# Performance work log

Measured on AMD Instinct MI355X. Metric: run time of the kernel, lower is better.

Reference implementation:

```python
import jax, jax.numpy as jnp
import numpy as np

H = 8          # num heads
LN_EPS = 1e-5  # torch LayerNorm default

_SHAPES = {
    'src': (1024, 8, 256), 'pos': (1024, 8, 256), 'query_embed': (80, 8, 256), 'cam_mask': (8, 80, 1024),
    'enc_qkv_w': (2, 768, 256), 'enc_qkv_b': (2, 768), 'enc_out_w': (2, 256, 256), 'enc_out_b': (2, 256),
    'enc_ln1_g': (2, 256), 'enc_ln1_b': (2, 256),
    'enc_ff1_w': (2, 2048, 256), 'enc_ff1_b': (2, 2048), 'enc_ff2_w': (2, 256, 2048), 'enc_ff2_b': (2, 256),
    'enc_ln2_g': (2, 256), 'enc_ln2_b': (2, 256),
    'dec_sa_qkv_w': (2, 768, 256), 'dec_sa_qkv_b': (2, 768), 'dec_sa_out_w': (2, 256, 256), 'dec_sa_out_b': (2, 256),
    'dec_ln1_g': (2, 256), 'dec_ln1_b': (2, 256),
    'dec_ca_qkv_w': (2, 768, 256), 'dec_ca_qkv_b': (2, 768), 'dec_ca_out_w': (2, 256, 256), 'dec_ca_out_b': (2, 256),
    'dec_ln2_g': (2, 256), 'dec_ln2_b': (2, 256),
    'dec_ff1_w': (2, 2048, 256), 'dec_ff1_b': (2, 2048), 'dec_ff2_w': (2, 256, 2048), 'dec_ff2_b': (2, 256),
    'dec_ln3_g': (2, 256), 'dec_ln3_b': (2, 256),
    'dec_norm_g': (256,), 'dec_norm_b': (256,),
}


def setup_inputs() -> dict:
    key = jax.random.key(0)
    out = {}
    for i, (name, sh) in enumerate(_SHAPES.items()):
        k = jax.random.fold_in(key, i)
        if name.endswith('_g'):
            out[name] = jnp.ones(sh, jnp.float32)
        elif name.endswith('ln1_b') or name.endswith('ln2_b') or name.endswith('ln3_b') or name == 'dec_norm_b':
            out[name] = jnp.zeros(sh, jnp.float32)
        else:
            scale = 1.0 if name in ('src', 'pos', 'query_embed', 'cam_mask') else 0.02
            out[name] = jax.random.normal(k, sh, dtype=jnp.float32) * scale
    return out


def layer_norm(x, g, b):
    mu = jnp.mean(x, axis=-1, keepdims=True)
    var = jnp.mean(jnp.square(x - mu), axis=-1, keepdims=True)
    return (x - mu) * jax.lax.rsqrt(var + LN_EPS) * g + b


def mha(q_in, k_in, v_in, qkv_w, qkv_b, out_w, out_b, bias=None):
    # q_in: [L,B,D], k_in/v_in: [S,B,D]; torch layout: projections are x @ W.T + b
    L, B, D = q_in.shape
    S = k_in.shape[0]
    hd = D // H
    wq, wk, wv = qkv_w[:D], qkv_w[D:2 * D], qkv_w[2 * D:]
    bq, bk, bv = qkv_b[:D], qkv_b[D:2 * D], qkv_b[2 * D:]
    q = (q_in @ wq.T + bq).reshape(L, B, H, hd).transpose(1, 2, 0, 3)  # [B,H,L,hd]
    k = (k_in @ wk.T + bk).reshape(S, B, H, hd).transpose(1, 2, 0, 3)  # [B,H,S,hd]
    v = (v_in @ wv.T + bv).reshape(S, B, H, hd).transpose(1, 2, 0, 3)
    logits = jnp.einsum('bhld,bhsd->bhls', q, k) * (1.0 / np.sqrt(hd))
    if bias is not None:
        logits = logits + bias[:, None, :, :]  # CAM bias broadcast over heads
    attn = jax.nn.softmax(logits, axis=-1)
    o = jnp.einsum('bhls,bhsd->bhld', attn, v).transpose(2, 0, 1, 3).reshape(L, B, D)
    return o @ out_w.T + out_b


def reference(src, pos, query_embed, cam_mask,
              enc_qkv_w, enc_qkv_b, enc_out_w, enc_out_b, enc_ln1_g, enc_ln1_b,
              enc_ff1_w, enc_ff1_b, enc_ff2_w, enc_ff2_b, enc_ln2_g, enc_ln2_b,
              dec_sa_qkv_w, dec_sa_qkv_b, dec_sa_out_w, dec_sa_out_b, dec_ln1_g, dec_ln1_b,
              dec_ca_qkv_w, dec_ca_qkv_b, dec_ca_out_w, dec_ca_out_b, dec_ln2_g, dec_ln2_b,
              dec_ff1_w, dec_ff1_b, dec_ff2_w, dec_ff2_b, dec_ln3_g, dec_ln3_b,
              dec_norm_g, dec_norm_b):
    n_enc = enc_qkv_w.shape[0]
    n_dec = dec_sa_qkv_w.shape[0]
    # --- encoder (post-norm DETR style, pos added to q,k) ---
    mem = src
    for i in range(n_enc):
        qk = mem + pos
        a = mha(qk, qk, mem, enc_qkv_w[i], enc_qkv_b[i], enc_out_w[i], enc_out_b[i])
        mem = layer_norm(mem + a, enc_ln1_g[i], enc_ln1_b[i])
        f = jax.nn.relu(mem @ enc_ff1_w[i].T + enc_ff1_b[i]) @ enc_ff2_w[i].T + enc_ff2_b[i]
        mem = layer_norm(mem + f, enc_ln2_g[i], enc_ln2_b[i])
    # --- decoder: tgt starts at zeros (Q2L), query_embed is query_pos ---
    tgt = jnp.zeros_like(query_embed)
    for i in range(n_dec):
        qk = tgt + query_embed
        sa = mha(qk, qk, tgt, dec_sa_qkv_w[i], dec_sa_qkv_b[i], dec_sa_out_w[i], dec_sa_out_b[i])
        tgt = layer_norm(tgt + sa, dec_ln1_g[i], dec_ln1_b[i])
        ca = mha(tgt + query_embed, mem + pos, mem,
                 dec_ca_qkv_w[i], dec_ca_qkv_b[i], dec_ca_out_w[i], dec_ca_out_b[i],
                 bias=cam_mask)  # MA: CAM-derived additive attention bias [B,L,S]
        tgt = layer_norm(tgt + ca, dec_ln2_g[i], dec_ln2_b[i])
        f = jax.nn.relu(tgt @ dec_ff1_w[i].T + dec_ff1_b[i]) @ dec_ff2_w[i].T + dec_ff2_b[i]
        tgt = layer_norm(tgt + f, dec_ln3_g[i], dec_ln3_b[i])
    out = layer_norm(tgt, dec_norm_g, dec_norm_b)
    return out[None]  # [1, L, B, D] as in TransformerDecoder's output.unsqueeze(0)
```

## Files before the change

### kernel.cpp

```cpp
#include <hip/hip_runtime.h>
#include <hip/hip_bf16.h>
#include <cstdint>
#include <cstddef>

typedef __hip_bfloat16 bf16;
typedef float f4 __attribute__((ext_vector_type(4)));
typedef float f32x4 __attribute__((ext_vector_type(4)));
typedef short s8v __attribute__((ext_vector_type(8)));
typedef unsigned short u16x4 __attribute__((ext_vector_type(4)));
typedef unsigned short u16x8 __attribute__((ext_vector_type(8)));

#define LN_EPS 1e-5f
#define LOG2E 1.4426950408889634f

#if __has_builtin(__builtin_amdgcn_exp2f)
__device__ __forceinline__ float EXP2(float x) { return __builtin_amdgcn_exp2f(x); }
#else
__device__ __forceinline__ float EXP2(float x) {
  float r; asm("v_exp_f32 %0, %1" : "=v"(r) : "v"(x)); return r;
}
#endif

__device__ __forceinline__ void async_cp16(const void* g, void* lds) {
  __builtin_amdgcn_global_load_lds(
      (const __attribute__((address_space(1))) unsigned int*)g,
      (__attribute__((address_space(3))) unsigned int*)lds, 16, 0, 0);
}

__device__ __forceinline__ uint32_t pkbf(float lo, float hi) {
#if __has_builtin(__builtin_amdgcn_perm)
  uint32_t l = __builtin_bit_cast(uint32_t, lo) + 0x8000u;
  uint32_t h = __builtin_bit_cast(uint32_t, hi) + 0x8000u;
  return __builtin_amdgcn_perm(h, l, 0x07060302u);
#else
  uint32_t l = __builtin_bit_cast(uint32_t, lo) + 0x8000u;
  uint32_t h = __builtin_bit_cast(uint32_t, hi) + 0x8000u;
  return (l >> 16) | (h & 0xFFFF0000u);
#endif
}

#define NCAST 17
struct CastArgs {
  const float* in[NCAST];
  bf16* out[NCAST];
  int end4[NCAST];
  int nseg;
};

__global__ __launch_bounds__(256) void cast_multi(CastArgs a, int total4) {
  int i = blockIdx.x * 256 + threadIdx.x;
  if (i >= total4) return;
  int s = 0;
  while (i >= a.end4[s]) ++s;
  int j = i - (s ? a.end4[s - 1] : 0);
  f4 v = ((const f4*)a.in[s])[j];
  u16x4 o;
#pragma unroll
  for (int c = 0; c < 4; ++c) {
    bf16 h = __float2bfloat16(v[c]);
    o[c] = *reinterpret_cast<unsigned short*>(&h);
  }
  ((u16x4*)a.out[s])[j] = o;
}

__global__ __launch_bounds__(256) void scale_f32_kernel(const float* __restrict__ in,
                                                        float* __restrict__ out,
                                                        float s, int n4) {
  int i = blockIdx.x * 256 + threadIdx.x;
  if (i < n4) {
    f4 v = ((const f4*)in)[i];
    ((f4*)out)[i] = v * s;
  }
}

__global__ __launch_bounds__(256) void add_bf16_kernel(const float* __restrict__ a,
                                                       const float* __restrict__ b,
                                                       bf16* __restrict__ out, int n4) {
  int i = blockIdx.x * 256 + threadIdx.x;
  if (i < n4) {
    f4 x = ((const f4*)a)[i];
    f4 y = ((const f4*)b)[i];
    u16x4 o;
#pragma unroll
    for (int j = 0; j < 4; ++j) {
      bf16 h = __float2bfloat16(x[j] + y[j]);
      o[j] = *reinterpret_cast<unsigned short*>(&h);
    }
    ((u16x4*)out)[i] = o;
  }
}

template <int TB, int MODE, int SPLITK>
__global__ __launch_bounds__(256, 2) void mfma_gemm(
    const bf16* __restrict__ A, const bf16* __restrict__ W,
    const float* __restrict__ bias, float* __restrict__ C,
    bf16* __restrict__ Cb, int M, int N, int K, int HL, float qscale) {
  constexpr int WM = TB / 2, WN = TB / 2;
  constexpr int MR = WM / 16, NR = WN / 16;
  constexpr int NCH = TB / 32;
  __shared__ __attribute__((aligned(16))) unsigned short SH[TB * 128];
  unsigned short (*As)[64] = (unsigned short(*)[64])SH;
  unsigned short (*Ws)[64] = (unsigned short(*)[64])(SH + TB * 64);
  const int tid = threadIdx.x;
  const int lane = tid & 63, wave = tid >> 6;
  const int wr = wave >> 1, wc = wave & 1;
  const int bm = blockIdx.x * TB, bn = blockIdx.y * TB;
  const int fr = lane & 15, fo = lane >> 4;
  const int srowi = lane >> 3;
  const int slot = lane & 7;
  const int gcol = (slot ^ srowi) * 8;

  const int kchunk = K / SPLITK;
  const int kbeg = (SPLITK > 1) ? blockIdx.z * kchunk : 0;

  f32x4 acc[MR][NR] = {};

  for (int k0 = kbeg; k0 < kbeg + kchunk; k0 += 64) {
    __syncthreads();
#pragma unroll
    for (int c = 0; c < NCH; ++c) {
      int rbase = wave * (TB / 4) + c * 8;
      int row = rbase + srowi;
      async_cp16(A + (size_t)(bm + row) * K + k0 + gcol, &As[rbase][0]);
      async_cp16(W + (size_t)(bn + row) * K + k0 + gcol, &Ws[rbase][0]);
    }
    __syncthreads();
#pragma unroll
    for (int ks = 0; ks < 2; ++ks) {
      s8v a[MR], b[NR];
#pragma unroll
      for (int mi = 0; mi < MR; ++mi) {
        int row = wr * WM + mi * 16 + fr;
        a[mi] = *(const s8v*)((const char*)&As[0][0] + row * 128 +
                              ((ks * 64 + fo * 16) ^ ((row & 7) << 4)));
      }
#pragma unroll
      for (int ni = 0; ni < NR; ++ni) {
        int row = wc * WN + ni * 16 + fr;
        b[ni] = *(const s8v*)((const char*)&Ws[0][0] + row * 128 +
                              ((ks * 64 + fo * 16) ^ ((row & 7) << 4)));
      }
#pragma unroll
      for (int mi = 0; mi < MR; ++mi)
#pragma unroll
        for (int ni = 0; ni < NR; ++ni)
          acc[mi][ni] = __builtin_amdgcn_mfma_f32_16x16x32_bf16(
              a[mi], b[ni], acc[mi][ni], 0, 0, 0);
    }
  }

  const int r0 = (lane >> 4) * 4;

  if (MODE == 5) {
    __syncthreads();
    unsigned short (*T)[72] = (unsigned short(*)[72])SH;
#pragma unroll
    for (int mi = 0; mi < MR; ++mi)
#pragma unroll
      for (int ni = 0; ni < NR; ++ni) {
        int colL = wc * WN + ni * 16 + fr;
        float bv = bias[bn + colL];
#pragma unroll
        for (int r = 0; r < 4; ++r) {
          int rowL = wr * WM + mi * 16 + r0 + r;
          bf16 hv = __float2bfloat16(acc[mi][ni][r] + bv);
          T[colL][rowL] = *(unsigned short*)&hv;
        }
      }
    __syncthreads();
    const int lbase = bm >> 3;
#pragma unroll
    for (int jj = 0; jj < 2; ++jj) {
      int cid = tid * 2 + jj;
      int colL = cid >> 3, bb = cid & 7;
      int c = bn + colL;
      int sec = c >> 8, hh = (c >> 5) & 7, d = c & 31;
      u16x8 v;
#pragma unroll
      for (int l = 0; l < 8; ++l) v[l] = T[colL][bb + 8 * l];
      *(u16x8*)(Cb + (size_t)sec * ((size_t)64 * 32 * HL) +
                ((size_t)(bb * 8 + hh) * 32 + d) * HL + lbase) = v;
    }
    return;
  }

  float* Cz = (MODE == 4) ? C + (size_t)blockIdx.z * M * N : C;
#pragma unroll
  for (int mi = 0; mi < MR; ++mi) {
#pragma unroll
    for (int ni = 0; ni < NR; ++ni) {
      int col = bn + wc * WN + ni * 16 + fr;
      float bv = (MODE == 4) ? 0.f : bias[col];
#pragma unroll
      for (int r = 0; r < 4; ++r) {
        int row = bm + wr * WM + mi * 16 + r0 + r;
        float t = acc[mi][ni][r] + bv;
        if (MODE == 2) t = fmaxf(t, 0.f);
        if (MODE == 0) {
          C[(size_t)row * N + col] = t;
        } else if (MODE == 4) {
          Cz[(size_t)row * N + col] = t;
        } else if (MODE == 3) {
          int l = row >> 3, bb = row & 7;
          int sec = col >> 8, hh = (col >> 5) & 7, d = col & 31;
          if (sec == 0) t *= qscale;
          Cb[(size_t)sec * ((size_t)64 * HL * 32) +
             ((size_t)(bb * 8 + hh) * HL + l) * 32 + d] = __float2bfloat16(t);
        } else {
          Cb[(size_t)row * N + col] = __float2bfloat16(t);
        }
      }
    }
  }
}

template <int HAS_BIAS, int PARTIAL, int NW>
__global__ __launch_bounds__(NW * 64, 3) void attn_mfma(
    const bf16* __restrict__ Qh, const bf16* __restrict__ Kh,
    const bf16* __restrict__ VhT, const float* __restrict__ bias,
    bf16* __restrict__ O, float* __restrict__ PO, float* __restrict__ PM,
    float* __restrict__ PL, int L, int S, int SC) {
  __shared__ __attribute__((aligned(16))) uint32_t Ps2[NW][2][16][36];
  const int tid = threadIdx.x;
  const int lane = tid & 63, wave = tid >> 6;
  const int fr = lane & 15, fo = lane >> 4;
  const int bh = blockIdx.x;
  const int b = bh >> 3, h = bh & 7;
  const int q0 = blockIdx.y * (NW * 16) + wave * 16;
  const int q = q0 + fr;

  const int cz = PARTIAL ? blockIdx.z : 0;
  const int sb = PARTIAL ? cz * SC : 0;
  const int se = PARTIAL ? min(S, sb + SC) : S;
  const int ng = (se - sb + 63) >> 6;

  s8v qf = {};
  if (q < L) qf = *(const s8v*)(Qh + ((size_t)bh * L + q) * 32 + fo * 8);

  const float* brow = nullptr;
  if (HAS_BIAS) brow = bias + ((size_t)b * L + (q < L ? q : L - 1)) * S;

  const bf16* Kbase = Kh + (size_t)bh * S * 32;
  const bf16* Vbase = VhT + (size_t)bh * 32 * S;

  float mA = -1e30f, lsA = 0.f, mB = -1e30f, lsB = 0.f;
  f32x4 oA[2] = {}, oB[2] = {};

  for (int g = 0; g < ng; g += 2) {
    const int sA = sb + g * 64, sB = sA + 64;

    s8v kA[4], kB[4], vA[2][2], vB[2][2];
#pragma unroll
    for (int kb = 0; kb < 4; ++kb) {
      kA[kb] = *(const s8v*)(Kbase + (size_t)(sA + kb * 16 + fr) * 32 + fo * 8);
      kB[kb] = *(const s8v*)(Kbase + (size_t)(sB + kb * 16 + fr) * 32 + fo * 8);
    }
#pragma unroll
    for (int dh = 0; dh < 2; ++dh)
#pragma unroll
      for (int ks = 0; ks < 2; ++ks) {
        vA[dh][ks] = *(const s8v*)(Vbase + (size_t)(dh * 16 + fr) * S +
                                   sA + ks * 32 + fo * 8);
        vB[dh][ks] = *(const s8v*)(Vbase + (size_t)(dh * 16 + fr) * S +
                                   sB + ks * 32 + fo * 8);
      }
    f4 bA[4], bB[4];
    if (HAS_BIAS) {
#pragma unroll
      for (int kb = 0; kb < 4; ++kb) {
        bA[kb] = *(const f4*)(brow + sA + kb * 16 + 4 * fo);
        bB[kb] = *(const f4*)(brow + sB + kb * 16 + 4 * fo);
      }
    }

    float lgA[16], lgB[16];
    __builtin_amdgcn_s_setprio(1);
#pragma unroll
    for (int kb = 0; kb < 4; ++kb) {
      f32x4 z = {};
      f32x4 sa = __builtin_amdgcn_mfma_f32_16x16x32_bf16(kA[kb], qf, z, 0, 0, 0);
#pragma unroll
      for (int r = 0; r < 4; ++r) lgA[kb * 4 + r] = sa[r];
    }
#pragma unroll
    for (int kb = 0; kb < 4; ++kb) {
      f32x4 z = {};
      f32x4 sa = __builtin_amdgcn_mfma_f32_16x16x32_bf16(kB[kb], qf, z, 0, 0, 0);
#pragma unroll
      for (int r = 0; r < 4; ++r) lgB[kb * 4 + r] = sa[r];
    }
    __builtin_amdgcn_s_setprio(0);
    if (HAS_BIAS) {
#pragma unroll
      for (int i = 0; i < 16; ++i) { lgA[i] += bA[i >> 2][i & 3]; lgB[i] += bB[i >> 2][i & 3]; }
    }
    if (sB + 64 > se) {
#pragma unroll
      for (int i = 0; i < 16; ++i) {
        int keyA = sA + (i >> 2) * 16 + 4 * fo + (i & 3);
        int keyB = sB + (i >> 2) * 16 + 4 * fo + (i & 3);
        if (keyA >= se) lgA[i] = -1e30f;
        if (keyB >= se) lgB[i] = -1e30f;
      }
    }

    float tA, tB;
    {
      float a0 = fmaxf(fmaxf(lgA[0], lgA[1]), fmaxf(lgA[2], lgA[3]));
      float a1 = fmaxf(fmaxf(lgA[4], lgA[5]), fmaxf(lgA[6], lgA[7]));
      float a2 = fmaxf(fmaxf(lgA[8], lgA[9]), fmaxf(lgA[10], lgA[11]));
      float a3 = fmaxf(fmaxf(lgA[12], lgA[13]), fmaxf(lgA[14], lgA[15]));
      tA = fmaxf(fmaxf(a0, a1), fmaxf(a2, a3));
      float b0 = fmaxf(fmaxf(lgB[0], lgB[1]), fmaxf(lgB[2], lgB[3]));
      float b1 = fmaxf(fmaxf(lgB[4], lgB[5]), fmaxf(lgB[6], lgB[7]));
      float b2 = fmaxf(fmaxf(lgB[8], lgB[9]), fmaxf(lgB[10], lgB[11]));
      float b3 = fmaxf(fmaxf(lgB[12], lgB[13]), fmaxf(lgB[14], lgB[15]));
      tB = fmaxf(fmaxf(b0, b1), fmaxf(b2, b3));
    }
    tA = fmaxf(tA, __shfl_xor(tA, 16));
    tB = fmaxf(tB, __shfl_xor(tB, 16));
    tA = fmaxf(tA, __shfl_xor(tA, 32));
    tB = fmaxf(tB, __shfl_xor(tB, 32));

    float nmA = fmaxf(mA, tA), nmB = fmaxf(mB, tB);
    float rsA = EXP2(mA - nmA), rsB = EXP2(mB - nmB);
    mA = nmA; mB = nmB;

    float psA = 0.f, psB = 0.f;
#pragma unroll
    for (int i = 0; i < 16; ++i) {
      lgA[i] = EXP2(lgA[i] - nmA); psA += lgA[i];
      lgB[i] = EXP2(lgB[i] - nmB); psB += lgB[i];
    }
    lsA = lsA * rsA + psA;
    lsB = lsB * rsB + psB;

#pragma unroll
    for (int kb = 0; kb < 4; ++kb) {
      uint32_t a0 = pkbf(lgA[kb * 4 + 0], lgA[kb * 4 + 1]);
      uint32_t a1 = pkbf(lgA[kb * 4 + 2], lgA[kb * 4 + 3]);
      *(uint64_t*)&Ps2[wave][0][fr][kb * 8 + 2 * fo] =
          (uint64_t)a0 | ((uint64_t)a1 << 32);
      uint32_t b0 = pkbf(lgB[kb * 4 + 0], lgB[kb * 4 + 1]);
      uint32_t b1 = pkbf(lgB[kb * 4 + 2], lgB[kb * 4 + 3]);
      *(uint64_t*)&Ps2[wave][1][fr][kb * 8 + 2 * fo] =
          (uint64_t)b0 | ((uint64_t)b1 << 32);
    }

#pragma unroll
    for (int r = 0; r < 4; ++r) {
      oA[0][r] *= rsA; oA[1][r] *= rsA;
      oB[0][r] *= rsB; oB[1][r] *= rsB;
    }
    s8v pA[2], pB[2];
#pragma unroll
    for (int ks = 0; ks < 2; ++ks) {
      pA[ks] = *(const s8v*)&Ps2[wave][0][fr][ks * 16 + 4 * fo];
      pB[ks] = *(const s8v*)&Ps2[wave][1][fr][ks * 16 + 4 * fo];
    }
    __builtin_amdgcn_s_setprio(1);
#pragma unroll
    for (int dh = 0; dh < 2; ++dh)
#pragma unroll
      for (int ks = 0; ks < 2; ++ks) {
        oA[dh] = __builtin_amdgcn_mfma_f32_16x16x32_bf16(vA[dh][ks], pA[ks], oA[dh], 0, 0, 0);
        oB[dh] = __builtin_amdgcn_mfma_f32_16x16x32_bf16(vB[dh][ks], pB[ks], oB[dh], 0, 0, 0);
      }
    __builtin_amdgcn_s_setprio(0);
  }

  float m = fmaxf(mA, mB);
  float wA = EXP2(mA - m), wB = EXP2(mB - m);
  float lsum = lsA * wA + lsB * wB;
  f32x4 oacc[2];
#pragma unroll
  for (int dh = 0; dh < 2; ++dh)
#pragma unroll
    for (int r = 0; r < 4; ++r)
      oacc[dh][r] = oA[dh][r] * wA + oB[dh][r] * wB;

  lsum += __shfl_xor(lsum, 16);
  lsum += __shfl_xor(lsum, 32);

  if (q < L) {
    if (PARTIAL) {
      size_t pi = ((size_t)cz * 64 + bh) * L + q;
      float* po = PO + pi * 32;
#pragma unroll
      for (int dh = 0; dh < 2; ++dh) {
        f4 t2;
#pragma unroll
        for (int r = 0; r < 4; ++r) t2[r] = oacc[dh][r];
        *(f4*)(po + dh * 16 + 4 * fo) = t2;
      }
      if (fo == 0) { PM[pi] = m; PL[pi] = lsum; }
    } else {
      float inv = 1.f / lsum;
      bf16* op = O + ((size_t)q * 8 + b) * 256 + h * 32;
#pragma unroll
      for (int dh = 0; dh < 2; ++dh) {
        uint32_t w0 = pkbf(oacc[dh][0] * inv, oacc[dh][1] * inv);
        uint32_t w1 = pkbf(oacc[dh][2] * inv, oacc[dh][3] * inv);
        *(uint32_t*)(op + dh * 16 + 4 * fo) = w0;
        *(uint32_t*)(op + dh * 16 + 4 * fo + 2) = w1;
      }
    }
  }
}

__global__ __launch_bounds__(256) void attn_combine(
    const float* __restrict__ PO, const float* __restrict__ PM,
    const float* __restrict__ PL, bf16* __restrict__ O, int L, int NC) {
  int gid = blockIdx.x * 256 + threadIdx.x;
  if (gid >= 64 * L * 32) return;
  int d = gid & 31;
  int rem = gid >> 5;
  int q = rem % L, bh = rem / L;
  int b = bh >> 3, h = bh & 7;
  float M = -1e30f;
  for (int c = 0; c < NC; ++c) M = fmaxf(M, PM[((size_t)c * 64 + bh) * L + q]);
  float lsum = 0.f, o = 0.f;
  for (int c = 0; c < NC; ++c) {
    size_t pi = ((size_t)c * 64 + bh) * L + q;
    float w = EXP2(PM[pi] - M);
    lsum += PL[pi] * w;
    o += PO[pi * 32 + d] * w;
  }
  O[((size_t)q * 8 + b) * 256 + h * 32 + d] = __float2bfloat16(o / lsum);
}

__global__ __launch_bounds__(256) void ln_kernel(
    const float* __restrict__ x, const float* __restrict__ res,
    const float* __restrict__ parts, int nparts, int pstride,
    const float* __restrict__ gbias,
    const float* __restrict__ g, const float* __restrict__ b,
    float* __restrict__ out, bf16* __restrict__ outb,
    const float* __restrict__ aux, bf16* __restrict__ auxb) {
  const int row = blockIdx.x, tid = threadIdx.x;
  size_t idx = (size_t)row * 256 + tid;
  float v = x[idx];
  if (res) v += res[idx];
  if (parts) {
    for (int z = 0; z < nparts; ++z) v += parts[(size_t)z * pstride + idx];
  }
  if (gbias) v += gbias[tid];
  float s = v, s2 = v * v;
#pragma unroll
  for (int off = 32; off >= 1; off >>= 1) {
    s += __shfl_down(s, off);
    s2 += __shfl_down(s2, off);
  }
  __shared__ float red[8];
  int wv = tid >> 6;
  if ((tid & 63) == 0) { red[wv] = s; red[4 + wv] = s2; }
  __syncthreads();
  if (tid == 0) {
    float ts = red[0] + red[1] + red[2] + red[3];
    float ts2 = red[4] + red[5] + red[6] + red[7];
    float mu = ts * (1.f / 256.f);
    float var = ts2 * (1.f / 256.f) - mu * mu;
    red[0] = mu;
    red[1] = rsqrtf(var + LN_EPS);
  }
  __syncthreads();
  float y = (v - red[0]) * red[1] * g[tid] + b[tid];
  if (out) out[idx] = y;
  if (outb) outb[idx] = __float2bfloat16(y);
  if (auxb) auxb[idx] = __float2bfloat16(y + aux[idx]);
}

extern "C" void kernel_launch(void* const* d_in, const int* in_sizes, int n_in,
                              void* d_out, int out_size, void* d_ws, size_t ws_size,
                              hipStream_t stream) {
  const float* src         = (const float*)d_in[0];
  const float* pos         = (const float*)d_in[1];
  const float* query_embed = (const float*)d_in[2];
  const float* cam_mask    = (const float*)d_in[3];
  const float* enc_qkv_w   = (const float*)d_in[4];
  const float* enc_qkv_b   = (const float*)d_in[5];
  const float* enc_out_w   = (const float*)d_in[6];
  const float* enc_out_b   = (const float*)d_in[7];
  const float* enc_ln1_g   = (const float*)d_in[8];
  const float* enc_ln1_b   = (const float*)d_in[9];
  const float* enc_ff1_w   = (const float*)d_in[10];
  const float* enc_ff1_b   = (const float*)d_in[11];
  const float* enc_ff2_w   = (const float*)d_in[12];
  const float* enc_ff2_b   = (const float*)d_in[13];
  const float* enc_ln2_g   = (const float*)d_in[14];
  const float* enc_ln2_b   = (const float*)d_in[15];
  const float* dec_sa_qkv_w= (const float*)d_in[16];
  const float* dec_sa_qkv_b= (const float*)d_in[17];
  const float* dec_sa_out_w= (const float*)d_in[18];
  const float* dec_sa_out_b= (const float*)d_in[19];
  const float* dec_ln1_g   = (const float*)d_in[20];
  const float* dec_ln1_b   = (const float*)d_in[21];
  const float* dec_ca_qkv_w= (const float*)d_in[22];
  const float* dec_ca_qkv_b= (const float*)d_in[23];
  const float* dec_ca_out_w= (const float*)d_in[24];
  const float* dec_ca_out_b= (const float*)d_in[25];
  const float* dec_ln2_g   = (const float*)d_in[26];
  const float* dec_ln2_b   = (const float*)d_in[27];
  const float* dec_ff1_w   = (const float*)d_in[28];
  const float* dec_ff1_b   = (const float*)d_in[29];
  const float* dec_ff2_w   = (const float*)d_in[30];
  const float* dec_ff2_b   = (const float*)d_in[31];
  const float* dec_ln3_g   = (const float*)d_in[32];
  const float* dec_ln3_b   = (const float*)d_in[33];
  const float* dec_norm_g  = (const float*)d_in[34];
  const float* dec_norm_b  = (const float*)d_in[35];

  size_t off = 0;
  char* base = (char*)d_ws;
  auto af = [&](size_t n) { float* p = (float*)(base + off); off += n * 4; return p; };
  auto ab = [&](size_t n) { bf16*  p = (bf16*)(base + off);  off += n * 2; return p; };

  float* mem  = af(2097152);
  float* r1   = af(2097152);
  float* PO   = af(8388608);
  float* pm   = af(262144);
  float* pl   = af(262144);
  float* cmlog= af(655360);
  float* pb   = af(1024);
  float* tgt  = af(163840);
  bf16* memb  = ab(2097152);
  bf16* qkb   = ab(2097152);
  bf16* aob   = ab(2097152);
  bf16* ffb   = ab(16777216);
  bf16* bufQ  = ab(4194304);
  bf16* bufK  = ab(4194304);
  bf16* bufV  = ab(4194304);
  bf16* bufVsa= ab(172032);
  bf16* tgtb  = ab(163840);
  bf16* tqkb  = ab(163840);
  bf16* taob  = ab(163840);
  bf16* qeb   = ab(163840);
  bf16* tffb  = ab(1310720);
  bf16* w_enc_qkv = ab(393216);
  bf16* w_enc_out = ab(131072);
  bf16* w_enc_ff1 = ab(1048576);
  bf16* w_enc_ff2 = ab(1048576);
  bf16* w_sa_qkv  = ab(393216);
  bf16* w_sa_out  = ab(131072);
  bf16* w_ca_q    = ab(131072);
  bf16* w_ca_kv   = ab(262144);
  bf16* w_ca_out  = ab(131072);
  bf16* w_dec_ff1 = ab(1048576);
  bf16* w_dec_ff2 = ab(1048576);

  const float qscale = 0.17677669529663687f * LOG2E;

  {
    CastArgs ca;
    const float* ins[NCAST] = {
        enc_qkv_w, enc_out_w, enc_ff1_w, enc_ff2_w,
        dec_sa_qkv_w, dec_sa_out_w,
        dec_ca_qkv_w,
        dec_ca_qkv_w + 65536,
        dec_ca_qkv_w + 131072,
        dec_ca_qkv_w + 196608,
        dec_ca_qkv_w + 262144,
        dec_ca_qkv_w + 327680,
        dec_ca_out_w, dec_ff1_w, dec_ff2_w, src, query_embed};
    bf16* outs[NCAST] = {
        w_enc_qkv, w_enc_out, w_enc_ff1, w_enc_ff2,
        w_sa_qkv, w_sa_out,
        w_ca_q,
        w_ca_kv,
        w_ca_kv + 131072,
        w_ca_q + 65536,
        w_ca_kv + 65536,
        w_ca_kv + 196608,
        w_ca_out, w_dec_ff1, w_dec_ff2, memb, qeb};
    int n4s[NCAST] = {98304, 32768, 262144, 262144, 98304, 32768,
                      16384, 16384, 16384, 16384, 16384, 16384,
                      32768, 262144, 262144, 524288, 40960};
    int acc = 0;
    for (int s = 0; s < NCAST; ++s) {
      ca.in[s] = ins[s]; ca.out[s] = outs[s];
      acc += n4s[s]; ca.end4[s] = acc;
    }
    ca.nseg = NCAST;
    cast_multi<<<(acc + 255) / 256, 256, 0, stream>>>(ca, acc);
  }
  scale_f32_kernel<<<640, 256, 0, stream>>>(cam_mask, cmlog, LOG2E, 163840);
  hipMemcpyAsync(mem, src, (size_t)2097152 * 4, hipMemcpyDeviceToDevice, stream);
  hipMemcpyAsync(pb,       dec_ca_qkv_b + 256,       1024, hipMemcpyDeviceToDevice, stream);
  hipMemcpyAsync(pb + 256, dec_ca_qkv_b + 768 + 256, 1024, hipMemcpyDeviceToDevice, stream);
  hipMemcpyAsync(pb + 512, dec_ca_qkv_b + 512,       1024, hipMemcpyDeviceToDevice, stream);
  hipMemcpyAsync(pb + 768, dec_ca_qkv_b + 768 + 512, 1024, hipMemcpyDeviceToDevice, stream);

  auto g64_head = [&](const bf16* A, const bf16* W, const float* bias, bf16* Cb,
                      int M, int N, int K, int HL, float qs) {
    mfma_gemm<64, 3, 1><<<dim3(M / 64, N / 64), 256, 0, stream>>>(
        A, W, bias, nullptr, Cb, M, N, K, HL, qs);
  };
  auto g64_headT = [&](const bf16* A, const bf16* W, const float* bias, bf16* Cb,
                       int M, int N, int K, int HL) {
    mfma_gemm<64, 5, 1><<<dim3(M / 64, N / 64), 256, 0, stream>>>(
        A, W, bias, nullptr, Cb, M, N, K, HL, 1.f);
  };
  auto g64_relu = [&](const bf16* A, const bf16* W, const float* bias, bf16* Cb,
                      int M, int N, int K) {
    mfma_gemm<64, 2, 1><<<dim3(M / 64, N / 64), 256, 0, stream>>>(
        A, W, bias, nullptr, Cb, M, N, K, 0, 1.f);
  };
  auto g128_relu = [&](const bf16* A, const bf16* W, const float* bias, bf16* Cb,
                       int M, int N, int K) {
    mfma_gemm<128, 2, 1><<<dim3(M / 128, N / 128), 256, 0, stream>>>(
        A, W, bias, nullptr, Cb, M, N, K, 0, 1.f);
  };

  add_bf16_kernel<<<2048, 256, 0, stream>>>(mem, pos, qkb, 524288);
  for (int i = 0; i < 2; ++i) {
    const bf16* wq = w_enc_qkv + (size_t)i * 196608;
    const float* qkvb = enc_qkv_b + (size_t)i * 768;
    g64_head(qkb, wq, qkvb, bufQ, 8192, 512, 256, 1024, qscale);
    g64_headT(memb, wq + 131072, qkvb + 512, bufV, 8192, 256, 256, 1024);
    attn_mfma<0, 0, 4><<<dim3(64, 16), 256, 0, stream>>>(
        bufQ, bufQ + 2097152, bufV, nullptr, aob, nullptr, nullptr, nullptr,
        1024, 1024, 0);
    mfma_gemm<64, 4, 2><<<dim3(128, 4, 2), 256, 0, stream>>>(
        aob, w_enc_out + (size_t)i * 65536, nullptr, PO, nullptr,
        8192, 256, 256, 0, 1.f);
    ln_kernel<<<8192, 256, 0, stream>>>(mem, nullptr, PO, 2, 2097152,
                                        enc_out_b + i * 256,
                                        enc_ln1_g + i * 256, enc_ln1_b + i * 256,
                                        mem, memb, nullptr, nullptr);
    g128_relu(memb, w_enc_ff1 + (size_t)i * 524288, enc_ff1_b + i * 2048, ffb,
              8192, 2048, 256);
    mfma_gemm<64, 4, 2><<<dim3(128, 4, 2), 256, 0, stream>>>(
        ffb, w_enc_ff2 + (size_t)i * 524288, nullptr, PO, nullptr,
        8192, 256, 2048, 0, 1.f);
    ln_kernel<<<8192, 256, 0, stream>>>(mem, nullptr, PO, 2, 2097152,
                                        enc_ff2_b + i * 256,
                                        enc_ln2_g + i * 256, enc_ln2_b + i * 256,
                                        mem, memb, pos, qkb);
  }

  hipMemsetAsync(tgt, 0, (size_t)163840 * 4, stream);
  hipMemsetAsync(tgtb, 0, (size_t)163840 * 2, stream);

  g64_head(qkb, w_ca_kv, pb, bufK, 8192, 512, 256, 1024, 1.f);
  g64_headT(memb, w_ca_kv + 131072, pb + 512, bufV, 8192, 512, 256, 1024);

  for (int i = 0; i < 2; ++i) {
    const bf16* wsa = w_sa_qkv + (size_t)i * 196608;
    const float* sab = dec_sa_qkv_b + (size_t)i * 768;
    const float* cab = dec_ca_qkv_b + (size_t)i * 768;
    const bf16* sa_in = (i == 0) ? qeb : tqkb;

    g64_head(sa_in, wsa, sab, bufQ, 640, 512, 256, 80, qscale);
    g64_headT(tgtb, wsa + 131072, sab + 512, bufVsa, 640, 256, 256, 80);
    attn_mfma<0, 0, 1><<<dim3(64, 5), 64, 0, stream>>>(
        bufQ, bufQ + 163840, bufVsa, nullptr, taob, nullptr, nullptr, nullptr,
        80, 80, 0);
    mfma_gemm<64, 4, 4><<<dim3(10, 4, 4), 256, 0, stream>>>(
        taob, w_sa_out + (size_t)i * 65536, nullptr, PO, nullptr,
        640, 256, 256, 0, 1.f);
    ln_kernel<<<640, 256, 0, stream>>>(tgt, nullptr, PO, 4, 163840,
                                       dec_sa_out_b + i * 256,
                                       dec_ln1_g + i * 256, dec_ln1_b + i * 256,
                                       tgt, tgtb, query_embed, tqkb);
    g64_head(tqkb, w_ca_q + (size_t)i * 65536, cab, bufQ, 640, 256, 256, 80, qscale);
    attn_mfma<1, 1, 1><<<dim3(64, 5, 8), 64, 0, stream>>>(
        bufQ, bufK + (size_t)i * 2097152, bufV + (size_t)i * 2097152, cmlog,
        nullptr, PO + 4194304, pm, pl, 80, 1024, 128);
    attn_combine<<<640, 256, 0, stream>>>(PO + 4194304, pm, pl, taob, 80, 8);
    mfma_gemm<64, 4, 4><<<dim3(10, 4, 4), 256, 0, stream>>>(
        taob, w_ca_out + (size_t)i * 65536, nullptr, PO, nullptr,
        640, 256, 256, 0, 1.f);
    ln_kernel<<<640, 256, 0, stream>>>(tgt, nullptr, PO, 4, 163840,
                                       dec_ca_out_b + i * 256,
                                       dec_ln2_g + i * 256, dec_ln2_b + i * 256,
                                       tgt, tgtb, nullptr, nullptr);
    g64_relu(tgtb, w_dec_ff1 + (size_t)i * 524288, dec_ff1_b + i * 2048, tffb,
             640, 2048, 256);
    mfma_gemm<64, 4, 4><<<dim3(10, 4, 4), 256, 0, stream>>>(
        tffb, w_dec_ff2 + (size_t)i * 524288, nullptr, PO, nullptr,
        640, 256, 2048, 0, 1.f);
    ln_kernel<<<640, 256, 0, stream>>>(tgt, nullptr, PO, 4, 163840,
                                       dec_ff2_b + i * 256,
                                       dec_ln3_g + i * 256, dec_ln3_b + i * 256,
                                       tgt, tgtb, query_embed, tqkb);
  }

  ln_kernel<<<640, 256, 0, stream>>>(tgt, nullptr, nullptr, 0, 0, nullptr,
                                     dec_norm_g, dec_norm_b,
                                     (float*)d_out, nullptr, nullptr, nullptr);
}
```

Measured before the change: 422.6 us.

## Fuse QK and V head projections into one launch; shortcut first decoder self-attention

A new GEMM mode 6 selects the A operand and output layout by column block, so the Q/K projection (head layout) and the V projection (transposed layout) run in a single launch for the encoder QKV, the cross-attention KV, and decoder layer-1 self-attention. For decoder layer 0, tgt is zero, so V equals its bias and attention output is the same for every query. The whole self-attention block therefore collapses to one row, out_w·bv + out_b followed by LayerNorm, which is broadcast to all rows. This removes several launches and the layer-0 self-attention GEMMs; it relies on the algebraic identity that holds for any inputs, since tgt starts at zero by model definition.

```diff
diff --git a/kernel.cpp b/kernel.cpp
--- a/kernel.cpp
+++ b/kernel.cpp
@@ -90,11 +90,56 @@
   }
 }
 
+__global__ __launch_bounds__(256) void sa0_row(
+    const float* __restrict__ Wo, const float* __restrict__ bv,
+    const float* __restrict__ bo, const float* __restrict__ g,
+    const float* __restrict__ b, float* __restrict__ row_out) {
+  const int j = threadIdx.x;
+  float acc = bo[j];
+  for (int k = 0; k < 256; k += 4) {
+    f4 w = *(const f4*)(Wo + (size_t)j * 256 + k);
+    f4 v = *(const f4*)(bv + k);
+    acc += w[0] * v[0] + w[1] * v[1] + w[2] * v[2] + w[3] * v[3];
+  }
+  float s = acc, s2 = acc * acc;
+#pragma unroll
+  for (int off = 32; off >= 1; off >>= 1) {
+    s += __shfl_down(s, off);
+    s2 += __shfl_down(s2, off);
+  }
+  __shared__ float red[8];
+  int wv = j >> 6;
+  if ((j & 63) == 0) { red[wv] = s; red[4 + wv] = s2; }
+  __syncthreads();
+  if (j == 0) {
+    float ts = red[0] + red[1] + red[2] + red[3];
+    float ts2 = red[4] + red[5] + red[6] + red[7];
+    float mu = ts * (1.f / 256.f);
+    float var = ts2 * (1.f / 256.f) - mu * mu;
+    red[0] = mu;
+    red[1] = rsqrtf(var + LN_EPS);
+  }
+  __syncthreads();
+  row_out[j] = (acc - red[0]) * red[1] * g[j] + b[j];
+}
+
+__global__ __launch_bounds__(256) void sa0_bcast(
+    const float* __restrict__ row, const float* __restrict__ qe,
+    float* __restrict__ tgt, bf16* __restrict__ tgtb, bf16* __restrict__ tqkb) {
+  const int r = blockIdx.x, j = threadIdx.x;
+  float y = row[j];
+  size_t idx = (size_t)r * 256 + j;
+  tgt[idx] = y;
+  tgtb[idx] = __float2bfloat16(y);
+  tqkb[idx] = __float2bfloat16(y + qe[idx]);
+}
+
 template <int TB, int MODE, int SPLITK>
 __global__ __launch_bounds__(256, 2) void mfma_gemm(
     const bf16* __restrict__ A, const bf16* __restrict__ W,
     const float* __restrict__ bias, float* __restrict__ C,
-    bf16* __restrict__ Cb, int M, int N, int K, int HL, float qscale) {
+    bf16* __restrict__ Cb, int M, int N, int K, int HL, float qscale,
+    const bf16* __restrict__ A2, bf16* __restrict__ Cb2, int nyA, int secV) {
   constexpr int WM = TB / 2, WN = TB / 2;
   constexpr int MR = WM / 16, NR = WN / 16;
   constexpr int NCH = TB / 32;
@@ -110,6 +155,8 @@
   const int slot = lane & 7;
   const int gcol = (slot ^ srowi) * 8;
 
+  const bf16* Aeff = (MODE == 6) ? (((int)blockIdx.y < nyA) ? A : A2) : A;
+
   const int kchunk = K / SPLITK;
   const int kbeg = (SPLITK > 1) ? blockIdx.z * kchunk : 0;
 
@@ -121,7 +168,7 @@
     for (int c = 0; c < NCH; ++c) {
       int rbase = wave * (TB / 4) + c * 8;
       int row = rbase + srowi;
-      async_cp16(A + (size_t)(bm + row) * K + k0 + gcol, &As[rbase][0]);
+      async_cp16(Aeff + (size_t)(bm + row) * K + k0 + gcol, &As[rbase][0]);
       async_cp16(W + (size_t)(bn + row) * K + k0 + gcol, &Ws[rbase][0]);
     }
     __syncthreads();
@@ -151,7 +198,7 @@
 
   const int r0 = (lane >> 4) * 4;
 
-  if (MODE == 5) {
+  if (MODE == 5 || (MODE == 6 && (bn >> 8) >= secV)) {
     __syncthreads();
     unsigned short (*T)[72] = (unsigned short(*)[72])SH;
 #pragma unroll
@@ -168,17 +215,19 @@
         }
       }
     __syncthreads();
+    bf16* Cv = (MODE == 6) ? Cb2 : Cb;
+    const int secBase = (MODE == 6) ? secV : 0;
     const int lbase = bm >> 3;
 #pragma unroll
     for (int jj = 0; jj < 2; ++jj) {
       int cid = tid * 2 + jj;
       int colL = cid >> 3, bb = cid & 7;
       int c = bn + colL;
-      int sec = c >> 8, hh = (c >> 5) & 7, d = c & 31;
+      int sec = (c >> 8) - secBase, hh = (c >> 5) & 7, d = c & 31;
       u16x8 v;
 #pragma unroll
       for (int l = 0; l < 8; ++l) v[l] = T[colL][bb + 8 * l];
-      *(u16x8*)(Cb + (size_t)sec * ((size_t)64 * 32 * HL) +
+      *(u16x8*)(Cv + (size_t)sec * ((size_t)64 * 32 * HL) +
                 ((size_t)(bb * 8 + hh) * 32 + d) * HL + lbase) = v;
     }
     return;
@@ -200,7 +249,7 @@
           C[(size_t)row * N + col] = t;
         } else if (MODE == 4) {
           Cz[(size_t)row * N + col] = t;
-        } else if (MODE == 3) {
+        } else if (MODE == 3 || MODE == 6) {
           int l = row >> 3, bb = row & 7;
           int sec = col >> 8, hh = (col >> 5) & 7, d = col & 31;
           if (sec == 0) t *= qscale;
@@ -515,12 +564,12 @@
   auto ab = [&](size_t n) { bf16*  p = (bf16*)(base + off);  off += n * 2; return p; };
 
   float* mem  = af(2097152);
-  float* r1   = af(2097152);
   float* PO   = af(8388608);
   float* pm   = af(262144);
   float* pl   = af(262144);
   float* cmlog= af(655360);
   float* pb   = af(1024);
+  float* row0 = af(256);
   float* tgt  = af(163840);
   bf16* memb  = ab(2097152);
   bf16* qkb   = ab(2097152);
@@ -592,36 +641,32 @@
   auto g64_head = [&](const bf16* A, const bf16* W, const float* bias, bf16* Cb,
                       int M, int N, int K, int HL, float qs) {
     mfma_gemm<64, 3, 1><<<dim3(M / 64, N / 64), 256, 0, stream>>>(
-        A, W, bias, nullptr, Cb, M, N, K, HL, qs);
-  };
-  auto g64_headT = [&](const bf16* A, const bf16* W, const float* bias, bf16* Cb,
-                       int M, int N, int K, int HL) {
-    mfma_gemm<64, 5, 1><<<dim3(M / 64, N / 64), 256, 0, stream>>>(
-        A, W, bias, nullptr, Cb, M, N, K, HL, 1.f);
+        A, W, bias, nullptr, Cb, M, N, K, HL, qs, nullptr, nullptr, 0, 0);
   };
   auto g64_relu = [&](const bf16* A, const bf16* W, const float* bias, bf16* Cb,
                       int M, int N, int K) {
     mfma_gemm<64, 2, 1><<<dim3(M / 64, N / 64), 256, 0, stream>>>(
-        A, W, bias, nullptr, Cb, M, N, K, 0, 1.f);
+        A, W, bias, nullptr, Cb, M, N, K, 0, 1.f, nullptr, nullptr, 0, 0);
   };
   auto g128_relu = [&](const bf16* A, const bf16* W, const float* bias, bf16* Cb,
                        int M, int N, int K) {
     mfma_gemm<128, 2, 1><<<dim3(M / 128, N / 128), 256, 0, stream>>>(
-        A, W, bias, nullptr, Cb, M, N, K, 0, 1.f);
+        A, W, bias, nullptr, Cb, M, N, K, 0, 1.f, nullptr, nullptr, 0, 0);
   };
 
   add_bf16_kernel<<<2048, 256, 0, stream>>>(mem, pos, qkb, 524288);
   for (int i = 0; i < 2; ++i) {
     const bf16* wq = w_enc_qkv + (size_t)i * 196608;
     const float* qkvb = enc_qkv_b + (size_t)i * 768;
-    g64_head(qkb, wq, qkvb, bufQ, 8192, 512, 256, 1024, qscale);
-    g64_headT(memb, wq + 131072, qkvb + 512, bufV, 8192, 256, 256, 1024);
+    mfma_gemm<64, 6, 1><<<dim3(128, 12), 256, 0, stream>>>(
+        qkb, wq, qkvb, nullptr, bufQ, 8192, 768, 256, 1024, qscale,
+        memb, bufV, 8, 2);
     attn_mfma<0, 0, 4><<<dim3(64, 16), 256, 0, stream>>>(
         bufQ, bufQ + 2097152, bufV, nullptr, aob, nullptr, nullptr, nullptr,
         1024, 1024, 0);
     mfma_gemm<64, 4, 2><<<dim3(128, 4, 2), 256, 0, stream>>>(
         aob, w_enc_out + (size_t)i * 65536, nullptr, PO, nullptr,
-        8192, 256, 256, 0, 1.f);
+        8192, 256, 256, 0, 1.f, nullptr, nullptr, 0, 0);
     ln_kernel<<<8192, 256, 0, stream>>>(mem, nullptr, PO, 2, 2097152,
                                         enc_out_b + i * 256,
                                         enc_ln1_g + i * 256, enc_ln1_b + i * 256,
@@ -630,37 +675,41 @@
               8192, 2048, 256);
     mfma_gemm<64, 4, 2><<<dim3(128, 4, 2), 256, 0, stream>>>(
         ffb, w_enc_ff2 + (size_t)i * 524288, nullptr, PO, nullptr,
-        8192, 256, 2048, 0, 1.f);
+        8192, 256, 2048, 0, 1.f, nullptr, nullptr, 0, 0);
     ln_kernel<<<8192, 256, 0, stream>>>(mem, nullptr, PO, 2, 2097152,
                                         enc_ff2_b + i * 256,
                                         enc_ln2_g + i * 256, enc_ln2_b + i * 256,
                                         mem, memb, pos, qkb);
   }
 
-  hipMemsetAsync(tgt, 0, (size_t)163840 * 4, stream);
-  hipMemsetAsync(tgtb, 0, (size_t)163840 * 2, stream);
-
-  g64_head(qkb, w_ca_kv, pb, bufK, 8192, 512, 256, 1024, 1.f);
-  g64_headT(memb, w_ca_kv + 131072, pb + 512, bufV, 8192, 512, 256, 1024);
+  mfma_gemm<64, 6, 1><<<dim3(128, 16), 256, 0, stream>>>(
+      qkb, w_ca_kv, pb, nullptr, bufK, 8192, 1024, 256, 1024, 1.f,
+      memb, bufV, 8, 2);
 
   for (int i = 0; i < 2; ++i) {
-    const bf16* wsa = w_sa_qkv + (size_t)i * 196608;
     const float* sab = dec_sa_qkv_b + (size_t)i * 768;
     const float* cab = dec_ca_qkv_b + (size_t)i * 768;
-    const bf16* sa_in = (i == 0) ? qeb : tqkb;
-
-    g64_head(sa_in, wsa, sab, bufQ, 640, 512, 256, 80, qscale);
-    g64_headT(tgtb, wsa + 131072, sab + 512, bufVsa, 640, 256, 256, 80);
-    attn_mfma<0, 0, 1><<<dim3(64, 5), 64, 0, stream>>>(
-        bufQ, bufQ + 163840, bufVsa, nullptr, taob, nullptr, nullptr, nullptr,
-        80, 80, 0);
-    mfma_gemm<64, 4, 4><<<dim3(10, 4, 4), 256, 0, stream>>>(
-        taob, w_sa_out + (size_t)i * 65536, nullptr, PO, nullptr,
-        640, 256, 256, 0, 1.f);
-    ln_kernel<<<640, 256, 0, stream>>>(tgt, nullptr, PO, 4, 163840,
-                                       dec_sa_out_b + i * 256,
-                                       dec_ln1_g + i * 256, dec_ln1_b + i * 256,
-                                       tgt, tgtb, query_embed, tqkb);
+
+    if (i == 0) {
+      sa0_row<<<1, 256, 0, stream>>>(dec_sa_out_w, dec_sa_qkv_b + 512,
+                                     dec_sa_out_b, dec_ln1_g, dec_ln1_b, row0);
+      sa0_bcast<<<640, 256, 0, stream>>>(row0, query_embed, tgt, tgtb, tqkb);
+    } else {
+      const bf16* wsa = w_sa_qkv + (size_t)i * 196608;
+      mfma_gemm<64, 6, 1><<<dim3(10, 12), 256, 0, stream>>>(
+          tqkb, wsa, sab, nullptr, bufQ, 640, 768, 256, 80, qscale,
+          tgtb, bufVsa, 8, 2);
+      attn_mfma<0, 0, 1><<<dim3(64, 5), 64, 0, stream>>>(
+          bufQ, bufQ + 163840, bufVsa, nullptr, taob, nullptr, nullptr, nullptr,
+          80, 80, 0);
+      mfma_gemm<64, 4, 4><<<dim3(10, 4, 4), 256, 0, stream>>>(
+          taob, w_sa_out + (size_t)i * 65536, nullptr, PO, nullptr,
+          640, 256, 256, 0, 1.f, nullptr, nullptr, 0, 0);
+      ln_kernel<<<640, 256, 0, stream>>>(tgt, nullptr, PO, 4, 163840,
+                                         dec_sa_out_b + i * 256,
+                                         dec_ln1_g + i * 256, dec_ln1_b + i * 256,
+                                         tgt, tgtb, query_embed, tqkb);
+    }
     g64_head(tqkb, w_ca_q + (size_t)i * 65536, cab, bufQ, 640, 256, 256, 80, qscale);
     attn_mfma<1, 1, 1><<<dim3(64, 5, 8), 64, 0, stream>>>(
         bufQ, bufK + (size_t)i * 2097152, bufV + (size_t)i * 2097152, cmlog,
@@ -668,7 +717,7 @@
     attn_combine<<<640, 256, 0, stream>>>(PO + 4194304, pm, pl, taob, 80, 8);
     mfma_gemm<64, 4, 4><<<dim3(10, 4, 4), 256, 0, stream>>>(
         taob, w_ca_out + (size_t)i * 65536, nullptr, PO, nullptr,
-        640, 256, 256, 0, 1.f);
+        640, 256, 256, 0, 1.f, nullptr, nullptr, 0, 0);
     ln_kernel<<<640, 256, 0, stream>>>(tgt, nullptr, PO, 4, 163840,
                                        dec_ca_out_b + i * 256,
                                        dec_ln2_g + i * 256, dec_ln2_b + i * 256,
@@ -677,7 +726,7 @@
              640, 2048, 256);
     mfma_gemm<64, 4, 4><<<dim3(10, 4, 4), 256, 0, stream>>>(
         tffb, w_dec_ff2 + (size_t)i * 524288, nullptr, PO, nullptr,
-        640, 256, 2048, 0, 1.f);
+        640, 256, 2048, 0, 1.f, nullptr, nullptr, 0, 0);
     ln_kernel<<<640, 256, 0, stream>>>(tgt, nullptr, PO, 4, 163840,
                                        dec_ff2_b + i * 256,
                                        dec_ln3_g + i * 256, dec_ln3_b + i * 256,
```

After: 396.8 us. -6.1%, faster.
